# Kernel optimization log

Measured on AMD Instinct MI355X. Metric: run time of the kernel, lower is better.

The kernel has to match this reference:

```python
import jax, jax.numpy as jnp
import numpy as np

B, D, L, E, H = 8192, 1024, 256, 16, 400

def setup_inputs() -> dict:
    key = jax.random.key(0)
    ks = jax.random.split(key, 6)
    s1 = 1.0 / np.sqrt(D)
    s2 = 1.0 / np.sqrt(H)
    return {
        "x": jax.random.normal(ks[0], (B, D), dtype=jnp.float32),
        "angle_idx": jax.random.randint(ks[1], (B,), 0, E, dtype=jnp.int64),
        "W1": jax.random.uniform(ks[2], (E, D, H), jnp.float32, -s1, s1),
        "b1": jax.random.uniform(ks[3], (E, H), jnp.float32, -s1, s1),
        "W2": jax.random.uniform(ks[4], (E, H, 2 * L), jnp.float32, -s2, s2),
        "b2": jax.random.uniform(ks[5], (E, 2 * L), jnp.float32, -s2, s2),
    }

def reference(x, angle_idx, W1, b1, W2, b2):
    # Dense all-experts compute, then per-sample select (jit-friendly MoE dispatch).
    # h1: [E, B, H]
    h1 = jax.nn.relu(jnp.einsum('bd,edh->ebh', x, W1) + b1[:, None, :])
    # h: [E, B, 2L]
    h = jnp.einsum('ebh,ehk->ebk', h1, W2) + b2[:, None, :]
    sel = h[angle_idx, jnp.arange(x.shape[0])]  # [B, 2L], each row from its routed expert
    half = sel.shape[1] // 2
    z_mu, z_logvar = sel[:, :half], sel[:, half:]
    return (z_mu, z_logvar)
```

## Files before the change

kernel.cpp:

```cpp
#include <hip/hip_runtime.h>
#include <hip/hip_bf16.h>
#include <cstdint>
#include <cstddef>

#define B_N 8192
#define D_K 1024
#define H_N 400
#define HP  416
#define K2_N 512
#define E_N 16
#define L_N 256
#define TM 64
#define PAD_ROWS (B_N + E_N * TM)
#define NTILES (PAD_ROWS / TM)

typedef short bf16x8 __attribute__((ext_vector_type(8)));
typedef float f32x4 __attribute__((ext_vector_type(4)));

#define GLDS(gp, lp) __builtin_amdgcn_global_load_lds( \
    (const __attribute__((address_space(1))) unsigned int*)(gp), \
    (__attribute__((address_space(3))) unsigned int*)(lp), 16, 0, 0)

static __device__ __forceinline__ unsigned short f2bf(float f) {
  union { float f; unsigned int u; } c; c.f = f;
  unsigned int u = c.u + 0x7fffu + ((c.u >> 16) & 1u);
  return (unsigned short)(u >> 16);
}
static __device__ __forceinline__ unsigned int pkbf(float a, float b) {
  union { __hip_bfloat162 v; unsigned int u; } c;
  c.v = __float22bfloat162_rn(make_float2(a, b));
  return c.u;
}

__global__ __launch_bounds__(256) void prep_kernel(const float* __restrict__ W1,
                                                   const float* __restrict__ W2,
                                                   const float* __restrict__ x,
                                                   const int* __restrict__ idx,
                                                   unsigned short* __restrict__ Wt1,
                                                   unsigned short* __restrict__ Wt2,
                                                   unsigned short* __restrict__ xc,
                                                   int* __restrict__ off_al,
                                                   int* __restrict__ order) {
  const int bid = blockIdx.x;
  const int t = threadIdx.x;
  if (bid < 2688) {
    __shared__ unsigned short Ls[64][72];
    const float* S; unsigned short* Dt; int K, N, Kd, Nd, k0, n0;
    if (bid < 1792) {
      int e = bid / 112, r = bid % 112;
      k0 = (r % 16) * 64; n0 = (r / 16) * 64;
      S = W1 + (size_t)e * D_K * H_N; Dt = Wt1 + (size_t)e * HP * D_K;
      K = D_K; N = H_N; Kd = D_K; Nd = HP;
    } else {
      int t2 = bid - 1792; int e = t2 / 56, r = t2 % 56;
      k0 = (r % 7) * 64; n0 = (r / 7) * 64;
      S = W2 + (size_t)e * H_N * K2_N; Dt = Wt2 + (size_t)e * K2_N * HP;
      K = H_N; N = K2_N; Kd = HP; Nd = K2_N;
    }
    const int kk = t >> 4;
    const int nn = (t & 15) * 4;
#pragma unroll
    for (int p = 0; p < 4; ++p) {
      int k = k0 + p * 16 + kk;
      int n = n0 + nn;
      float4 v = make_float4(0.f, 0.f, 0.f, 0.f);
      if (k < K && n + 3 < N) v = *(const float4*)(S + (size_t)k * N + n);
      Ls[nn + 0][p * 16 + kk] = f2bf(v.x);
      Ls[nn + 1][p * 16 + kk] = f2bf(v.y);
      Ls[nn + 2][p * 16 + kk] = f2bf(v.z);
      Ls[nn + 3][p * 16 + kk] = f2bf(v.w);
    }
    __syncthreads();
    const int n2 = t >> 3;
    const int ch = t & 7;
#pragma unroll
    for (int p = 0; p < 2; ++p) {
      int n = n0 + p * 32 + n2;
      int k = k0 + ch * 8;
      if (n < Nd && k < Kd)
        *(uint4*)(Dt + (size_t)n * Kd + k) = *(const uint4*)&Ls[p * 32 + n2][ch * 8];
    }
  } else if (bid < 3200) {
    const int xb = bid - 2688;
    const float* S = x + (size_t)xb * 16 * D_K;
    unsigned short* Dp = xc + (size_t)xb * 16 * D_K;
#pragma unroll
    for (int i = 0; i < 16; ++i) {
      float4 v = *(const float4*)(S + i * D_K + t * 4);
      uint2 o; o.x = pkbf(v.x, v.y); o.y = pkbf(v.z, v.w);
      *(uint2*)(Dp + i * D_K + t * 4) = o;
    }
  } else {
    __shared__ int cnt[E_N];
    __shared__ int curS[E_N];
    *(uint2*)(xc + (size_t)B_N * D_K + t * 4) = make_uint2(0, 0);
    if (t < E_N) cnt[t] = 0;
    __syncthreads();
    for (int b = t; b < B_N; b += 256) atomicAdd(&cnt[idx[b]], 1);
    __syncthreads();
    if (t == 0) {
      int acc = 0;
      for (int e = 0; e < E_N; ++e) {
        off_al[e] = acc; curS[e] = acc;
        acc += ((cnt[e] + TM - 1) / TM) * TM;
      }
      off_al[E_N] = acc;
    }
    for (int i = t; i < PAD_ROWS; i += 256) order[i] = -1;
    __syncthreads();
    for (int b = t; b < B_N; b += 256) {
      int e = idx[b];
      order[atomicAdd(&curS[e], 1)] = b;
    }
  }
}

__global__ __launch_bounds__(256) void gemm1_kernel(const unsigned short* __restrict__ xc,
                                                    const unsigned short* __restrict__ Wt1,
                                                    const float* __restrict__ b1,
                                                    const int* __restrict__ off_al,
                                                    const int* __restrict__ order,
                                                    unsigned short* __restrict__ h1buf) {
  __shared__ unsigned short As[2][64 * 32];
  __shared__ unsigned short Bs[2][112 * 32];
  __shared__ int offs[E_N + 1];
  __shared__ int rowidx[TM];
  const int tid = threadIdx.x;
  const int m0 = blockIdx.x * TM;
  const int nb = blockIdx.y;
  const int tstart = (nb < 2) ? 7 * nb : 14 + 6 * (nb - 2);
  const int tcnt   = (nb < 2) ? 7 : 6;
  if (tid <= E_N) offs[tid] = off_al[tid];
  if (tid < TM) {
    int s = order[m0 + tid];
    rowidx[tid] = (s < 0) ? B_N : s;
  }
  __syncthreads();
  if (m0 >= offs[E_N]) return;
  int e = 0;
  while (m0 >= offs[e + 1]) ++e;
  const unsigned short* Wt1e = Wt1 + (size_t)e * HP * D_K;

  const int l = tid & 63, w = tid >> 6;
  const int r4 = l >> 2;
  const int sg = (r4 ^ (r4 >> 2)) & 3;
  const int g8 = ((l & 3) ^ sg) * 8;
  const int tl1 = w + 4;
  const unsigned short* gA  = xc + (size_t)rowidx[16 * w + r4] * D_K + g8;
  const unsigned short* gB0 = Wt1e + (size_t)((tstart + w) * 16 + r4) * D_K + g8;
  const unsigned short* gB1 = Wt1e + (size_t)((tstart + tl1) * 16 + r4) * D_K + g8;

  const int ln = l & 15, q = l >> 4;
  const int sr = (ln ^ (ln >> 2)) & 3;
  const int cq = (q ^ sr) * 8;

  f32x4 acc[4][2] = {};

  GLDS(gA, &As[0][16 * w * 32]);
  GLDS(gB0, &Bs[0][16 * w * 32]);
  if (tl1 < tcnt) GLDS(gB1, &Bs[0][16 * tl1 * 32]);

  for (int k0 = 0; k0 < D_K; k0 += 32) {
    const int cur = (k0 >> 5) & 1;
    const int nxt = cur ^ 1;
    __syncthreads();
    if (k0 + 32 < D_K) {
      GLDS(gA + k0 + 32, &As[nxt][16 * w * 32]);
      GLDS(gB0 + k0 + 32, &Bs[nxt][16 * w * 32]);
      if (tl1 < tcnt) GLDS(gB1 + k0 + 32, &Bs[nxt][16 * tl1 * 32]);
    }
    bf16x8 af[4];
#pragma unroll
    for (int i = 0; i < 4; ++i)
      af[i] = *(const bf16x8*)&As[cur][(16 * i + ln) * 32 + cq];
    {
      bf16x8 bf0 = *(const bf16x8*)&Bs[cur][(16 * w + ln) * 32 + cq];
#pragma unroll
      for (int i = 0; i < 4; ++i)
        acc[i][0] = __builtin_amdgcn_mfma_f32_16x16x32_bf16(af[i], bf0, acc[i][0], 0, 0, 0);
    }
    if (tl1 < tcnt) {
      bf16x8 bf1 = *(const bf16x8*)&Bs[cur][(16 * tl1 + ln) * 32 + cq];
#pragma unroll
      for (int i = 0; i < 4; ++i)
        acc[i][1] = __builtin_amdgcn_mfma_f32_16x16x32_bf16(af[i], bf1, acc[i][1], 0, 0, 0);
    }
  }

#pragma unroll
  for (int t = 0; t < 2; ++t) {
    const int tl = w + 4 * t;
    if (tl < tcnt) {
      const int n = (tstart + tl) * 16 + ln;
      if (n < H_N) {
        const float bias = b1[e * H_N + n];
#pragma unroll
        for (int i = 0; i < 4; ++i)
#pragma unroll
          for (int r = 0; r < 4; ++r) {
            const int m = m0 + 16 * i + 4 * q + r;
            h1buf[(size_t)m * HP + n] = f2bf(fmaxf(acc[i][t][r] + bias, 0.f));
          }
      }
    }
  }
  if (nb == 3 && tid < TM) {
    uint4 z = make_uint4(0, 0, 0, 0);
    *(uint4*)&h1buf[(size_t)(m0 + tid) * HP + 400] = z;
    *(uint4*)&h1buf[(size_t)(m0 + tid) * HP + 408] = z;
  }
}

__global__ __launch_bounds__(256) void gemm2_kernel(const unsigned short* __restrict__ h1buf,
                                                    const unsigned short* __restrict__ Wt2,
                                                    const float* __restrict__ b2,
                                                    const int* __restrict__ off_al,
                                                    const int* __restrict__ order,
                                                    float* __restrict__ out) {
  __shared__ unsigned short As[2][64 * 32];
  __shared__ unsigned short Bs[2][128 * 32];
  __shared__ int offs[E_N + 1];
  __shared__ int rowidx[TM];
  const int tid = threadIdx.x;
  const int m0 = blockIdx.x * TM;
  const int nbase = blockIdx.y * 128;
  if (tid <= E_N) offs[tid] = off_al[tid];
  if (tid < TM) rowidx[tid] = order[m0 + tid];
  __syncthreads();
  if (m0 >= offs[E_N]) return;
  int e = 0;
  while (m0 >= offs[e + 1]) ++e;
  const unsigned short* Wt2e = Wt2 + (size_t)e * K2_N * HP;

  const int l = tid & 63, w = tid >> 6;
  const int r4 = l >> 2;
  const int sg = (r4 ^ (r4 >> 2)) & 3;
  const int g8 = ((l & 3) ^ sg) * 8;
  const int tl1 = w + 4;
  const unsigned short* gA  = h1buf + (size_t)(m0 + 16 * w + r4) * HP + g8;
  const unsigned short* gB0 = Wt2e + (size_t)(nbase + 16 * w + r4) * HP + g8;
  const unsigned short* gB1 = Wt2e + (size_t)(nbase + 16 * tl1 + r4) * HP + g8;

  const int ln = l & 15, q = l >> 4;
  const int sr = (ln ^ (ln >> 2)) & 3;
  const int cq = (q ^ sr) * 8;

  f32x4 acc[4][2] = {};

  GLDS(gA, &As[0][16 * w * 32]);
  GLDS(gB0, &Bs[0][16 * w * 32]);
  GLDS(gB1, &Bs[0][16 * tl1 * 32]);

  for (int k0 = 0; k0 < HP; k0 += 32) {
    const int cur = (k0 >> 5) & 1;
    const int nxt = cur ^ 1;
    __syncthreads();
    if (k0 + 32 < HP) {
      GLDS(gA + k0 + 32, &As[nxt][16 * w * 32]);
      GLDS(gB0 + k0 + 32, &Bs[nxt][16 * w * 32]);
      GLDS(gB1 + k0 + 32, &Bs[nxt][16 * tl1 * 32]);
    }
    bf16x8 af[4];
#pragma unroll
    for (int i = 0; i < 4; ++i)
      af[i] = *(const bf16x8*)&As[cur][(16 * i + ln) * 32 + cq];
#pragma unroll
    for (int t = 0; t < 2; ++t) {
      const int tl = w + 4 * t;
      bf16x8 bfr = *(const bf16x8*)&Bs[cur][(16 * tl + ln) * 32 + cq];
#pragma unroll
      for (int i = 0; i < 4; ++i)
        acc[i][t] = __builtin_amdgcn_mfma_f32_16x16x32_bf16(af[i], bfr, acc[i][t], 0, 0, 0);
    }
  }

#pragma unroll
  for (int t = 0; t < 2; ++t) {
    const int tl = w + 4 * t;
    const int n = nbase + 16 * tl + ln;
    const float bias = b2[e * K2_N + n];
#pragma unroll
    for (int i = 0; i < 4; ++i)
#pragma unroll
      for (int r = 0; r < 4; ++r) {
        const int s = rowidx[16 * i + 4 * q + r];
        if (s >= 0) {
          const float v = acc[i][t][r] + bias;
          if (n < L_N) out[(size_t)s * L_N + n] = v;
          else         out[(size_t)(B_N + s) * L_N + (n - L_N)] = v;
        }
      }
  }
}

extern "C" void kernel_launch(void* const* d_in, const int* in_sizes, int n_in,
                              void* d_out, int out_size, void* d_ws, size_t ws_size,
                              hipStream_t stream) {
  const float* x   = (const float*)d_in[0];
  const int*   idx = (const int*)d_in[1];
  const float* W1  = (const float*)d_in[2];
  const float* b1  = (const float*)d_in[3];
  const float* W2  = (const float*)d_in[4];
  const float* b2  = (const float*)d_in[5];
  float* out = (float*)d_out;

  char* ws = (char*)d_ws;
  int* off_al = (int*)(ws + 0);
  int* order  = (int*)(ws + 2240);
  unsigned short* xc  = (unsigned short*)(ws + 39104);
  unsigned short* h1  = (unsigned short*)(ws + 16818368);
  unsigned short* Wt1 = (unsigned short*)(ws + 24486080);
  unsigned short* Wt2 = (unsigned short*)(ws + 38117568);

  prep_kernel<<<3201, 256, 0, stream>>>(W1, W2, x, idx, Wt1, Wt2, xc, off_al, order);
  gemm1_kernel<<<dim3(NTILES, 4), 256, 0, stream>>>(xc, Wt1, b1, off_al, order, h1);
  gemm2_kernel<<<dim3(NTILES, 4), 256, 0, stream>>>(h1, Wt2, b2, off_al, order, out);
}
```

Measured before the change: 175.4 us.

## Parallelize expert routing histogram and scatter across blocks with wave-aggregated atomics

The single-block routing step inside the prep kernel (histogram, prefix offsets, scatter of row indices) is replaced. Thirty-two prep blocks now each build a partial histogram and clear their slice of the order array. A new 32-block scatter kernel sums those histograms, computes the padded offsets, and assigns slots using wave ballots with one global atomic per expert per wave. The weight-transpose loop also issues all four float4 loads before converting and storing them. This removes a serial tail block that could lengthen the prep kernel, but adds an extra kernel launch and makes the row order within an expert non-deterministic.

```diff
diff --git a/kernel.cpp b/kernel.cpp
--- a/kernel.cpp
+++ b/kernel.cpp
@@ -39,7 +39,8 @@
                                                    unsigned short* __restrict__ Wt1,
                                                    unsigned short* __restrict__ Wt2,
                                                    unsigned short* __restrict__ xc,
-                                                   int* __restrict__ off_al,
+                                                   int* __restrict__ hist,
+                                                   int* __restrict__ cur0,
                                                    int* __restrict__ order) {
   const int bid = blockIdx.x;
   const int t = threadIdx.x;
@@ -59,16 +60,20 @@
     }
     const int kk = t >> 4;
     const int nn = (t & 15) * 4;
+    float4 v[4];
 #pragma unroll
     for (int p = 0; p < 4; ++p) {
       int k = k0 + p * 16 + kk;
       int n = n0 + nn;
-      float4 v = make_float4(0.f, 0.f, 0.f, 0.f);
-      if (k < K && n + 3 < N) v = *(const float4*)(S + (size_t)k * N + n);
-      Ls[nn + 0][p * 16 + kk] = f2bf(v.x);
-      Ls[nn + 1][p * 16 + kk] = f2bf(v.y);
-      Ls[nn + 2][p * 16 + kk] = f2bf(v.z);
-      Ls[nn + 3][p * 16 + kk] = f2bf(v.w);
+      v[p] = make_float4(0.f, 0.f, 0.f, 0.f);
+      if (k < K && n + 3 < N) v[p] = *(const float4*)(S + (size_t)k * N + n);
+    }
+#pragma unroll
+    for (int p = 0; p < 4; ++p) {
+      Ls[nn + 0][p * 16 + kk] = f2bf(v[p].x);
+      Ls[nn + 1][p * 16 + kk] = f2bf(v[p].y);
+      Ls[nn + 2][p * 16 + kk] = f2bf(v[p].z);
+      Ls[nn + 3][p * 16 + kk] = f2bf(v[p].w);
     }
     __syncthreads();
     const int n2 = t >> 3;
@@ -91,28 +96,64 @@
       *(uint2*)(Dp + i * D_K + t * 4) = o;
     }
   } else {
-    __shared__ int cnt[E_N];
-    __shared__ int curS[E_N];
-    *(uint2*)(xc + (size_t)B_N * D_K + t * 4) = make_uint2(0, 0);
-    if (t < E_N) cnt[t] = 0;
-    __syncthreads();
-    for (int b = t; b < B_N; b += 256) atomicAdd(&cnt[idx[b]], 1);
-    __syncthreads();
-    if (t == 0) {
-      int acc = 0;
-      for (int e = 0; e < E_N; ++e) {
-        off_al[e] = acc; curS[e] = acc;
-        acc += ((cnt[e] + TM - 1) / TM) * TM;
-      }
-      off_al[E_N] = acc;
-    }
-    for (int i = t; i < PAD_ROWS; i += 256) order[i] = -1;
-    __syncthreads();
-    for (int b = t; b < B_N; b += 256) {
-      int e = idx[b];
-      order[atomicAdd(&curS[e], 1)] = b;
-    }
-  }
+    __shared__ int h[E_N];
+    const int hb = bid - 3200;
+    if (t < E_N) h[t] = 0;
+    __syncthreads();
+    atomicAdd(&h[idx[hb * 256 + t]], 1);
+    __syncthreads();
+    if (t < E_N) hist[hb * E_N + t] = h[t];
+    const int base = hb * (PAD_ROWS / 32);
+    for (int i = base + t; i < base + PAD_ROWS / 32; i += 256) order[i] = -1;
+    if (hb == 0) {
+      if (t < E_N) cur0[t] = 0;
+      *(uint2*)(xc + (size_t)B_N * D_K + t * 4) = make_uint2(0, 0);
+    }
+  }
+}
+
+__global__ __launch_bounds__(256) void scatter_kernel(const int* __restrict__ idx,
+                                                      const int* __restrict__ hist,
+                                                      int* __restrict__ cur0,
+                                                      int* __restrict__ off_al,
+                                                      int* __restrict__ order) {
+  __shared__ int offsL[E_N];
+  const int t = threadIdx.x;
+  __shared__ int cnt[E_N];
+  if (t < E_N) {
+    int s = 0;
+    for (int b = 0; b < 32; ++b) s += hist[b * E_N + t];
+    cnt[t] = s;
+  }
+  __syncthreads();
+  if (t == 0) {
+    int acc = 0;
+    for (int e = 0; e < E_N; ++e) {
+      offsL[e] = acc;
+      if (blockIdx.x == 0) off_al[e] = acc;
+      acc += ((cnt[e] + TM - 1) / TM) * TM;
+    }
+    if (blockIdx.x == 0) off_al[E_N] = acc;
+  }
+  __syncthreads();
+  const int b = blockIdx.x * 256 + t;
+  const int e = idx[b];
+  const int lane = t & 63;
+  const unsigned long long below = (lane == 63) ? ~0ull >> 1 : ((1ull << lane) - 1);
+  int slot = 0;
+#pragma unroll
+  for (int ee = 0; ee < E_N; ++ee) {
+    unsigned long long m = __ballot(e == ee);
+    if (m != 0) {
+      int leader = __ffsll((unsigned long long)m) - 1;
+      int c = __popcll(m);
+      int wb = 0;
+      if (lane == leader) wb = atomicAdd(&cur0[ee], c);
+      wb = __shfl(wb, leader, 64);
+      if (e == ee) slot = offsL[ee] + wb + __popcll(m & below);
+    }
+  }
+  order[slot] = b;
 }
 
 __global__ __launch_bounds__(256) void gemm1_kernel(const unsigned short* __restrict__ xc,
@@ -306,13 +347,16 @@
 
   char* ws = (char*)d_ws;
   int* off_al = (int*)(ws + 0);
+  int* cur0   = (int*)(ws + 128);
+  int* hist   = (int*)(ws + 192);
   int* order  = (int*)(ws + 2240);
   unsigned short* xc  = (unsigned short*)(ws + 39104);
   unsigned short* h1  = (unsigned short*)(ws + 16818368);
   unsigned short* Wt1 = (unsigned short*)(ws + 24486080);
   unsigned short* Wt2 = (unsigned short*)(ws + 38117568);
 
-  prep_kernel<<<3201, 256, 0, stream>>>(W1, W2, x, idx, Wt1, Wt2, xc, off_al, order);
+  prep_kernel<<<3232, 256, 0, stream>>>(W1, W2, x, idx, Wt1, Wt2, xc, hist, cur0, order);
+  scatter_kernel<<<32, 256, 0, stream>>>(idx, hist, cur0, off_al, order);
   gemm1_kernel<<<dim3(NTILES, 4), 256, 0, stream>>>(xc, Wt1, b1, off_al, order, h1);
   gemm2_kernel<<<dim3(NTILES, 4), 256, 0, stream>>>(h1, Wt2, b2, off_al, order, out);
 }
```

After: 187.7 us. 1.07x slower.

## Parallelize expert routing via histogram kernel and shrink GEMM N-tiles for occupancy

Applied to the files above, without the earlier changes.

Expert counting and ordering used to run in a single block looping over all 8192 rows. A small histogram kernel now runs first, and 32 prep blocks each scatter their own 256 rows using prefix offsets, which removes the single-block serial tail. Both GEMMs drop to one 16-column N-tile per wave with more blocks in the grid, which lowers LDS and register use and raises parallelism, at the cost of reloading the A tile more often. Padded rows are now found from the stored counts instead of by pre-filling order with -1, and the loads in the weight transpose are batched ahead of the stores.

```diff
diff --git a/kernel.cpp b/kernel.cpp
--- a/kernel.cpp
+++ b/kernel.cpp
@@ -32,14 +32,27 @@
   return c.u;
 }
 
+__global__ __launch_bounds__(256) void hist_kernel(const int* __restrict__ idx,
+                                                   int* __restrict__ hist) {
+  __shared__ int h[E_N];
+  const int t = threadIdx.x;
+  if (t < E_N) h[t] = 0;
+  __syncthreads();
+  atomicAdd(&h[idx[blockIdx.x * 256 + t]], 1);
+  __syncthreads();
+  if (t < E_N) hist[blockIdx.x * E_N + t] = h[t];
+}
+
 __global__ __launch_bounds__(256) void prep_kernel(const float* __restrict__ W1,
                                                    const float* __restrict__ W2,
                                                    const float* __restrict__ x,
                                                    const int* __restrict__ idx,
+                                                   const int* __restrict__ hist,
                                                    unsigned short* __restrict__ Wt1,
                                                    unsigned short* __restrict__ Wt2,
                                                    unsigned short* __restrict__ xc,
                                                    int* __restrict__ off_al,
+                                                   int* __restrict__ cnt_al,
                                                    int* __restrict__ order) {
   const int bid = blockIdx.x;
   const int t = threadIdx.x;
@@ -59,16 +72,20 @@
     }
     const int kk = t >> 4;
     const int nn = (t & 15) * 4;
+    float4 v[4];
 #pragma unroll
     for (int p = 0; p < 4; ++p) {
       int k = k0 + p * 16 + kk;
       int n = n0 + nn;
-      float4 v = make_float4(0.f, 0.f, 0.f, 0.f);
-      if (k < K && n + 3 < N) v = *(const float4*)(S + (size_t)k * N + n);
-      Ls[nn + 0][p * 16 + kk] = f2bf(v.x);
-      Ls[nn + 1][p * 16 + kk] = f2bf(v.y);
-      Ls[nn + 2][p * 16 + kk] = f2bf(v.z);
-      Ls[nn + 3][p * 16 + kk] = f2bf(v.w);
+      v[p] = make_float4(0.f, 0.f, 0.f, 0.f);
+      if (k < K && n + 3 < N) v[p] = *(const float4*)(S + (size_t)k * N + n);
+    }
+#pragma unroll
+    for (int p = 0; p < 4; ++p) {
+      Ls[nn + 0][p * 16 + kk] = f2bf(v[p].x);
+      Ls[nn + 1][p * 16 + kk] = f2bf(v[p].y);
+      Ls[nn + 2][p * 16 + kk] = f2bf(v[p].z);
+      Ls[nn + 3][p * 16 + kk] = f2bf(v[p].w);
     }
     __syncthreads();
     const int n2 = t >> 3;
@@ -91,27 +108,38 @@
       *(uint2*)(Dp + i * D_K + t * 4) = o;
     }
   } else {
-    __shared__ int cnt[E_N];
-    __shared__ int curS[E_N];
-    *(uint2*)(xc + (size_t)B_N * D_K + t * 4) = make_uint2(0, 0);
-    if (t < E_N) cnt[t] = 0;
-    __syncthreads();
-    for (int b = t; b < B_N; b += 256) atomicAdd(&cnt[idx[b]], 1);
+    const int hb = bid - 3200;
+    __shared__ int totL[E_N], preL[E_N], offsL[E_N], curL[E_N];
+    if (t < E_N) {
+      int pre = 0, tot = 0;
+      for (int b = 0; b < 32; ++b) {
+        int h = hist[b * E_N + t];
+        if (b < hb) pre += h;
+        tot += h;
+      }
+      totL[t] = tot; preL[t] = pre;
+    }
     __syncthreads();
     if (t == 0) {
       int acc = 0;
       for (int e = 0; e < E_N; ++e) {
-        off_al[e] = acc; curS[e] = acc;
-        acc += ((cnt[e] + TM - 1) / TM) * TM;
+        offsL[e] = acc;
+        if (hb == 0) off_al[e] = acc;
+        acc += ((totL[e] + TM - 1) / TM) * TM;
       }
-      off_al[E_N] = acc;
-    }
-    for (int i = t; i < PAD_ROWS; i += 256) order[i] = -1;
-    __syncthreads();
-    for (int b = t; b < B_N; b += 256) {
-      int e = idx[b];
-      order[atomicAdd(&curS[e], 1)] = b;
-    }
+      if (hb == 0) off_al[E_N] = acc;
+    }
+    __syncthreads();
+    if (t < E_N) {
+      curL[t] = offsL[t] + preL[t];
+      if (hb == 0) cnt_al[t] = totL[t];
+    }
+    __syncthreads();
+    const int b = hb * 256 + t;
+    const int e = idx[b];
+    const int slot = atomicAdd(&curL[e], 1);
+    order[slot] = b;
+    if (hb == 0) *(uint2*)(xc + (size_t)B_N * D_K + t * 4) = make_uint2(0, 0);
   }
 }
 
@@ -119,46 +147,46 @@
                                                     const unsigned short* __restrict__ Wt1,
                                                     const float* __restrict__ b1,
                                                     const int* __restrict__ off_al,
+                                                    const int* __restrict__ cnt_al,
                                                     const int* __restrict__ order,
                                                     unsigned short* __restrict__ h1buf) {
   __shared__ unsigned short As[2][64 * 32];
-  __shared__ unsigned short Bs[2][112 * 32];
+  __shared__ unsigned short Bs[2][64 * 32];
   __shared__ int offs[E_N + 1];
   __shared__ int rowidx[TM];
   const int tid = threadIdx.x;
   const int m0 = blockIdx.x * TM;
   const int nb = blockIdx.y;
-  const int tstart = (nb < 2) ? 7 * nb : 14 + 6 * (nb - 2);
-  const int tcnt   = (nb < 2) ? 7 : 6;
+  const int tstart = (nb < 5) ? 4 * nb : 20 + 3 * (nb - 5);
+  const int tcnt   = (nb < 5) ? 4 : 3;
   if (tid <= E_N) offs[tid] = off_al[tid];
-  if (tid < TM) {
-    int s = order[m0 + tid];
-    rowidx[tid] = (s < 0) ? B_N : s;
-  }
   __syncthreads();
   if (m0 >= offs[E_N]) return;
   int e = 0;
   while (m0 >= offs[e + 1]) ++e;
+  if (tid < TM) {
+    const bool valid = (m0 + tid) < (offs[e] + cnt_al[e]);
+    rowidx[tid] = valid ? order[m0 + tid] : B_N;
+  }
+  __syncthreads();
   const unsigned short* Wt1e = Wt1 + (size_t)e * HP * D_K;
 
   const int l = tid & 63, w = tid >> 6;
   const int r4 = l >> 2;
   const int sg = (r4 ^ (r4 >> 2)) & 3;
   const int g8 = ((l & 3) ^ sg) * 8;
-  const int tl1 = w + 4;
-  const unsigned short* gA  = xc + (size_t)rowidx[16 * w + r4] * D_K + g8;
-  const unsigned short* gB0 = Wt1e + (size_t)((tstart + w) * 16 + r4) * D_K + g8;
-  const unsigned short* gB1 = Wt1e + (size_t)((tstart + tl1) * 16 + r4) * D_K + g8;
+  const bool wact = (w < tcnt);
+  const unsigned short* gA = xc + (size_t)rowidx[16 * w + r4] * D_K + g8;
+  const unsigned short* gB = Wt1e + (size_t)((tstart + w) * 16 + r4) * D_K + g8;
 
   const int ln = l & 15, q = l >> 4;
   const int sr = (ln ^ (ln >> 2)) & 3;
   const int cq = (q ^ sr) * 8;
 
-  f32x4 acc[4][2] = {};
+  f32x4 acc[4] = {};
 
   GLDS(gA, &As[0][16 * w * 32]);
-  GLDS(gB0, &Bs[0][16 * w * 32]);
-  if (tl1 < tcnt) GLDS(gB1, &Bs[0][16 * tl1 * 32]);
+  if (wact) GLDS(gB, &Bs[0][16 * w * 32]);
 
   for (int k0 = 0; k0 < D_K; k0 += 32) {
     const int cur = (k0 >> 5) & 1;
@@ -166,48 +194,32 @@
     __syncthreads();
     if (k0 + 32 < D_K) {
       GLDS(gA + k0 + 32, &As[nxt][16 * w * 32]);
-      GLDS(gB0 + k0 + 32, &Bs[nxt][16 * w * 32]);
-      if (tl1 < tcnt) GLDS(gB1 + k0 + 32, &Bs[nxt][16 * tl1 * 32]);
-    }
-    bf16x8 af[4];
-#pragma unroll
-    for (int i = 0; i < 4; ++i)
-      af[i] = *(const bf16x8*)&As[cur][(16 * i + ln) * 32 + cq];
-    {
-      bf16x8 bf0 = *(const bf16x8*)&Bs[cur][(16 * w + ln) * 32 + cq];
+      if (wact) GLDS(gB + k0 + 32, &Bs[nxt][16 * w * 32]);
+    }
+    if (wact) {
+      bf16x8 af[4];
 #pragma unroll
       for (int i = 0; i < 4; ++i)
-        acc[i][0] = __builtin_amdgcn_mfma_f32_16x16x32_bf16(af[i], bf0, acc[i][0], 0, 0, 0);
-    }
-    if (tl1 < tcnt) {
-      bf16x8 bf1 = *(const bf16x8*)&Bs[cur][(16 * tl1 + ln) * 32 + cq];
+        af[i] = *(const bf16x8*)&As[cur][(16 * i + ln) * 32 + cq];
+      bf16x8 bfr = *(const bf16x8*)&Bs[cur][(16 * w + ln) * 32 + cq];
 #pragma unroll
       for (int i = 0; i < 4; ++i)
-        acc[i][1] = __builtin_amdgcn_mfma_f32_16x16x32_bf16(af[i], bf1, acc[i][1], 0, 0, 0);
-    }
-  }
-
-#pragma unroll
-  for (int t = 0; t < 2; ++t) {
-    const int tl = w + 4 * t;
-    if (tl < tcnt) {
-      const int n = (tstart + tl) * 16 + ln;
-      if (n < H_N) {
-        const float bias = b1[e * H_N + n];
-#pragma unroll
-        for (int i = 0; i < 4; ++i)
-#pragma unroll
-          for (int r = 0; r < 4; ++r) {
-            const int m = m0 + 16 * i + 4 * q + r;
-            h1buf[(size_t)m * HP + n] = f2bf(fmaxf(acc[i][t][r] + bias, 0.f));
-          }
-      }
-    }
-  }
-  if (nb == 3 && tid < TM) {
-    uint4 z = make_uint4(0, 0, 0, 0);
-    *(uint4*)&h1buf[(size_t)(m0 + tid) * HP + 400] = z;
-    *(uint4*)&h1buf[(size_t)(m0 + tid) * HP + 408] = z;
+        acc[i] = __builtin_amdgcn_mfma_f32_16x16x32_bf16(af[i], bfr, acc[i], 0, 0, 0);
+    }
+  }
+
+  if (wact) {
+    const int n = (tstart + w) * 16 + ln;
+    if (n < H_N) {
+      const float bias = b1[e * H_N + n];
+#pragma unroll
+      for (int i = 0; i < 4; ++i)
+#pragma unroll
+        for (int r = 0; r < 4; ++r) {
+          const int m = m0 + 16 * i + 4 * q + r;
+          h1buf[(size_t)m * HP + n] = f2bf(fmaxf(acc[i][r] + bias, 0.f));
+        }
+    }
   }
 }
 
@@ -215,41 +227,43 @@
                                                     const unsigned short* __restrict__ Wt2,
                                                     const float* __restrict__ b2,
                                                     const int* __restrict__ off_al,
+                                                    const int* __restrict__ cnt_al,
                                                     const int* __restrict__ order,
                                                     float* __restrict__ out) {
   __shared__ unsigned short As[2][64 * 32];
-  __shared__ unsigned short Bs[2][128 * 32];
+  __shared__ unsigned short Bs[2][64 * 32];
   __shared__ int offs[E_N + 1];
   __shared__ int rowidx[TM];
   const int tid = threadIdx.x;
   const int m0 = blockIdx.x * TM;
-  const int nbase = blockIdx.y * 128;
+  const int nb = blockIdx.y;
   if (tid <= E_N) offs[tid] = off_al[tid];
-  if (tid < TM) rowidx[tid] = order[m0 + tid];
   __syncthreads();
   if (m0 >= offs[E_N]) return;
   int e = 0;
   while (m0 >= offs[e + 1]) ++e;
+  if (tid < TM) {
+    const bool valid = (m0 + tid) < (offs[e] + cnt_al[e]);
+    rowidx[tid] = valid ? order[m0 + tid] : -1;
+  }
+  __syncthreads();
   const unsigned short* Wt2e = Wt2 + (size_t)e * K2_N * HP;
 
   const int l = tid & 63, w = tid >> 6;
   const int r4 = l >> 2;
   const int sg = (r4 ^ (r4 >> 2)) & 3;
   const int g8 = ((l & 3) ^ sg) * 8;
-  const int tl1 = w + 4;
-  const unsigned short* gA  = h1buf + (size_t)(m0 + 16 * w + r4) * HP + g8;
-  const unsigned short* gB0 = Wt2e + (size_t)(nbase + 16 * w + r4) * HP + g8;
-  const unsigned short* gB1 = Wt2e + (size_t)(nbase + 16 * tl1 + r4) * HP + g8;
+  const unsigned short* gA = h1buf + (size_t)(m0 + 16 * w + r4) * HP + g8;
+  const unsigned short* gB = Wt2e + (size_t)((4 * nb + w) * 16 + r4) * HP + g8;
 
   const int ln = l & 15, q = l >> 4;
   const int sr = (ln ^ (ln >> 2)) & 3;
   const int cq = (q ^ sr) * 8;
 
-  f32x4 acc[4][2] = {};
+  f32x4 acc[4] = {};
 
   GLDS(gA, &As[0][16 * w * 32]);
-  GLDS(gB0, &Bs[0][16 * w * 32]);
-  GLDS(gB1, &Bs[0][16 * tl1 * 32]);
+  GLDS(gB, &Bs[0][16 * w * 32]);
 
   for (int k0 = 0; k0 < HP; k0 += 32) {
     const int cur = (k0 >> 5) & 1;
@@ -257,40 +271,31 @@
     __syncthreads();
     if (k0 + 32 < HP) {
       GLDS(gA + k0 + 32, &As[nxt][16 * w * 32]);
-      GLDS(gB0 + k0 + 32, &Bs[nxt][16 * w * 32]);
-      GLDS(gB1 + k0 + 32, &Bs[nxt][16 * tl1 * 32]);
+      GLDS(gB + k0 + 32, &Bs[nxt][16 * w * 32]);
     }
     bf16x8 af[4];
 #pragma unroll
     for (int i = 0; i < 4; ++i)
       af[i] = *(const bf16x8*)&As[cur][(16 * i + ln) * 32 + cq];
-#pragma unroll
-    for (int t = 0; t < 2; ++t) {
-      const int tl = w + 4 * t;
-      bf16x8 bfr = *(const bf16x8*)&Bs[cur][(16 * tl + ln) * 32 + cq];
-#pragma unroll
-      for (int i = 0; i < 4; ++i)
-        acc[i][t] = __builtin_amdgcn_mfma_f32_16x16x32_bf16(af[i], bfr, acc[i][t], 0, 0, 0);
-    }
-  }
-
-#pragma unroll
-  for (int t = 0; t < 2; ++t) {
-    const int tl = w + 4 * t;
-    const int n = nbase + 16 * tl + ln;
-    const float bias = b2[e * K2_N + n];
+    bf16x8 bfr = *(const bf16x8*)&Bs[cur][(16 * w + ln) * 32 + cq];
 #pragma unroll
     for (int i = 0; i < 4; ++i)
-#pragma unroll
-      for (int r = 0; r < 4; ++r) {
-        const int s = rowidx[16 * i + 4 * q + r];
-        if (s >= 0) {
-          const float v = acc[i][t][r] + bias;
-          if (n < L_N) out[(size_t)s * L_N + n] = v;
-          else         out[(size_t)(B_N + s) * L_N + (n - L_N)] = v;
-        }
+      acc[i] = __builtin_amdgcn_mfma_f32_16x16x32_bf16(af[i], bfr, acc[i], 0, 0, 0);
+  }
+
+  const int n = (4 * nb + w) * 16 + ln;
+  const float bias = b2[e * K2_N + n];
+#pragma unroll
+  for (int i = 0; i < 4; ++i)
+#pragma unroll
+    for (int r = 0; r < 4; ++r) {
+      const int s = rowidx[16 * i + 4 * q + r];
+      if (s >= 0) {
+        const float v = acc[i][r] + bias;
+        if (n < L_N) out[(size_t)s * L_N + n] = v;
+        else         out[(size_t)(B_N + s) * L_N + (n - L_N)] = v;
       }
-  }
+    }
 }
 
 extern "C" void kernel_launch(void* const* d_in, const int* in_sizes, int n_in,
@@ -306,13 +311,17 @@
 
   char* ws = (char*)d_ws;
   int* off_al = (int*)(ws + 0);
+  int* cnt_al = (int*)(ws + 128);
+  int* hist   = (int*)(ws + 192);
   int* order  = (int*)(ws + 2240);
   unsigned short* xc  = (unsigned short*)(ws + 39104);
   unsigned short* h1  = (unsigned short*)(ws + 16818368);
   unsigned short* Wt1 = (unsigned short*)(ws + 24486080);
   unsigned short* Wt2 = (unsigned short*)(ws + 38117568);
 
-  prep_kernel<<<3201, 256, 0, stream>>>(W1, W2, x, idx, Wt1, Wt2, xc, off_al, order);
-  gemm1_kernel<<<dim3(NTILES, 4), 256, 0, stream>>>(xc, Wt1, b1, off_al, order, h1);
-  gemm2_kernel<<<dim3(NTILES, 4), 256, 0, stream>>>(h1, Wt2, b2, off_al, order, out);
-}
+  hist_kernel<<<32, 256, 0, stream>>>(idx, hist);
+  prep_kernel<<<3232, 256, 0, stream>>>(W1, W2, x, idx, hist, Wt1, Wt2, xc,
+                                        off_al, cnt_al, order);
+  gemm1_kernel<<<dim3(NTILES, 7), 256, 0, stream>>>(xc, Wt1, b1, off_al, cnt_al, order, h1);
+  gemm2_kernel<<<dim3(NTILES, 8), 256, 0, stream>>>(h1, Wt2, b2, off_al, cnt_al, order, out);
+}
```

Measured after the change: 160.6 us. 8.5% less time.
